# Performance work log

Hardware: AMD Instinct MI355X
Metric: run time of the kernel (lower is better)

## Reference

```python
import jax, jax.numpy as jnp
import numpy as np

MAX_DISP = 4  # matches init_kwargs


def setup_inputs() -> dict:
    key = jax.random.key(0)
    k1, k2 = jax.random.split(key)
    fmap1 = jax.random.normal(k1, (8, 256, 64, 128), dtype=jnp.float32)
    fmap2 = jax.random.normal(k2, (8, 256, 64, 128), dtype=jnp.float32)
    return {"fmap1": fmap1, "fmap2": fmap2}


def reference(fmap1, fmap2):
    # corr(x,y,dx,dy) = sum_c fmap1[c,y,x] * fmap2[c,y+dy,x+dx]
    pad = MAX_DISP
    B, C, H, W = fmap1.shape
    f2p = jnp.pad(fmap2, ((0, 0), (0, 0), (pad, pad), (pad, pad)))
    side = 2 * pad + 1  # 9 -> 81 displacements total
    # Loop over the small fixed set of 81 static displacements; each term is a
    # fused elementwise-multiply + channel reduction (einsum over c).
    corrs = [
        jnp.einsum('bchw,bchw->bhw', fmap1, f2p[:, :, y0:y0 + H, x0:x0 + W])
        for y0 in range(side)
        for x0 in range(side)
    ]
    return jnp.stack(corrs, axis=1)  # (B, 81, H, W)
```

## Files before the change

### kernel.cpp

```cpp
#include <hip/hip_runtime.h>


namespace {
constexpr int B_ = 8, C_ = 256, H_ = 64, W_ = 128;
constexpr int SIDE = 9, ND = 81, PAD = 4;
constexpr int HW = H_ * W_;
constexpr int CB = 32;
constexpr int HP = 72, WP = 144;
constexpr size_t BWS_U4 = (size_t)B_ * CB * HP * WP;
constexpr size_t BWS_BYTES = BWS_U4 * 16;
}

typedef __attribute__((ext_vector_type(8))) short short8;
typedef __attribute__((ext_vector_type(4))) float float4v;

__device__ __forceinline__ unsigned bf16rne(float f) {
  unsigned u = __float_as_uint(f);
  return (u + 0x7fffu + ((u >> 16) & 1u)) >> 16;
}
__device__ __forceinline__ unsigned packbf2(float lo, float hi) {
  return bf16rne(lo) | (bf16rne(hi) << 16);
}

__global__ __launch_bounds__(256)
void cvt_f2(const float* __restrict__ f2, uint4* __restrict__ bws) {
  const int tid = blockIdx.x * 256 + threadIdx.x;
  const int xq = tid % (WP / 4);
  int r = tid / (WP / 4);
  const int yp = r % HP;
  r /= HP;
  const int cb = r % CB;
  const int b = r / CB;

  uint4 o[4] = {};
  const int yg = yp - PAD;
  const int x = xq * 4 - PAD;
  if (yg >= 0 && yg < H_ && x >= 0 && x + 3 < W_) {
    const float* s = f2 + ((size_t)(b * C_ + cb * 8) * H_ + yg) * W_ + x;
    float vv[8][4];
#pragma unroll
    for (int e = 0; e < 8; ++e) {
      const float4 t = *(const float4*)(s + (size_t)e * HW);
      vv[e][0] = t.x; vv[e][1] = t.y; vv[e][2] = t.z; vv[e][3] = t.w;
    }
#pragma unroll
    for (int p = 0; p < 4; ++p) {
      o[p].x = packbf2(vv[0][p], vv[1][p]);
      o[p].y = packbf2(vv[2][p], vv[3][p]);
      o[p].z = packbf2(vv[4][p], vv[5][p]);
      o[p].w = packbf2(vv[6][p], vv[7][p]);
    }
  }
  uint4* d = bws + ((size_t)(b * CB + cb) * HP + yp) * WP + xq * 4;
#pragma unroll
  for (int p = 0; p < 4; ++p) d[p] = o[p];
}

__global__ __launch_bounds__(256, 4)
void corr_mfma(const float* __restrict__ f1, const uint4* __restrict__ bws,
               float* __restrict__ out) {
  const int t = threadIdx.x;
  const int lane = t & 63;
  const int wv = t >> 6;
  const int jm = blockIdx.x * 2 + (wv >> 1);
  const int half = wv & 1;
  const int y = blockIdx.y;
  const int b = blockIdx.z;
  const int v = lane & 15;
  const int q = lane >> 4;
  const int dyb = half * 5;
  const int ndy = 5 - half;

  float4v acc0[5], acc1[5];
#pragma unroll
  for (int i = 0; i < 5; ++i) {
    acc0[i] = (float4v){0.f, 0.f, 0.f, 0.f};
    acc1[i] = (float4v){0.f, 0.f, 0.f, 0.f};
  }

  const float* a_base = f1 + ((size_t)(b * C_ + q * 8) * H_ + y) * W_ + 16 * jm + v;
  const uint4* b_base = bws + ((size_t)(b * CB) + q) * (HP * WP) + 16 * jm + v;

  for (int ch = 0; ch < 8; ++ch) {
    float av[8];
#pragma unroll
    for (int j = 0; j < 8; ++j) av[j] = a_base[(size_t)(ch * 32 + j) * HW];
    uint4 afu;
    afu.x = packbf2(av[0], av[1]);
    afu.y = packbf2(av[2], av[3]);
    afu.z = packbf2(av[4], av[5]);
    afu.w = packbf2(av[6], av[7]);
    const short8 af = __builtin_bit_cast(short8, afu);

    const uint4* bc = b_base + (size_t)(ch * 4) * (HP * WP) + (size_t)(y + dyb) * WP;
#pragma unroll
    for (int i = 0; i < 5; ++i) {
      if (i < ndy) {
        const uint4* bp = bc + (size_t)i * WP;
        const short8 b0 = __builtin_bit_cast(short8, bp[0]);
        const short8 b1 = __builtin_bit_cast(short8, bp[16]);
        acc0[i] = __builtin_amdgcn_mfma_f32_16x16x32_bf16(af, b0, acc0[i], 0, 0, 0);
        acc1[i] = __builtin_amdgcn_mfma_f32_16x16x32_bf16(af, b1, acc1[i], 0, 0, 0);
      }
    }
  }

#pragma unroll
  for (int i = 0; i < 5; ++i) {
    if (i < ndy) {
      const int dy = dyb + i;
#pragma unroll
      for (int r = 0; r < 4; ++r) {
        const int m = q * 4 + r;
        const int x = 16 * jm + m;
        const int dx0 = v - m;
        if (dx0 >= 0 && dx0 <= 8)
          out[(((size_t)b * ND + dy * SIDE + dx0) * H_ + y) * W_ + x] = acc0[i][r];
        const int dx1 = v - m + 16;
        if (dx1 <= 8)
          out[(((size_t)b * ND + dy * SIDE + dx1) * H_ + y) * W_ + x] = acc1[i][r];
      }
    }
  }
}

namespace fb {
constexpr int PXS = 20, F2PX = 80, F1PX = 64, KC = 32, NCH = C_ / KC;
constexpr int F2U = SIDE * (F2PX / 4) * (KC / 2);
constexpr int F1U = (F1PX / 4) * (KC / 2);
constexpr int NU = F2U + F1U;
}

__global__ __launch_bounds__(512, 4)
void corr_fallback(const float* __restrict__ f1, const float* __restrict__ f2,
                   float* __restrict__ out) {
  using namespace fb;
  __shared__ __align__(16) unsigned f2s[SIDE * F2PX * PXS];
  __shared__ __align__(16) unsigned f1s[F1PX * PXS];

  const int t = threadIdx.x;
  const int bx = blockIdx.x, by = blockIdx.y, b = blockIdx.z;
  const int x0B = bx * 64;
  const int lane = t & 63, wv = t >> 6;
  const int wt = wv >> 1, half = wv & 1;
  const int dyb = half * 5, ndy = 5 - half;
  const int v = lane & 15, q = lane >> 4;

  float4v acc0[5], acc1[5];
#pragma unroll
  for (int i = 0; i < 5; ++i) {
    acc0[i] = (float4v){0.f, 0.f, 0.f, 0.f};
    acc1[i] = (float4v){0.f, 0.f, 0.f, 0.f};
  }
  const float* __restrict__ f1b = f1 + (size_t)b * C_ * HW;
  const float* __restrict__ f2b = f2 + (size_t)b * C_ * HW;

  for (int ch = 0; ch < NCH; ++ch) {
    const int c0 = ch * KC;
    if (ch) __syncthreads();
    for (int u = t; u < NU; u += 512) {
      if (u < F2U) {
        const int cp = u & 15;
        const int rp = u >> 4;
        const int pxq = rp % 20;
        const int r = rp / 20;
        const int yg = by + r - PAD;
        const int xb = x0B - PAD + pxq * 4;
        float4 va = make_float4(0.f, 0.f, 0.f, 0.f), vb = va;
        if (yg >= 0 && yg < H_ && xb >= 0 && xb <= W_ - 4) {
          const float* p = f2b + ((size_t)(c0 + 2 * cp) * H_ + yg) * W_ + xb;
          va = *(const float4*)p;
          vb = *(const float4*)(p + HW);
        }
        unsigned* d = &f2s[(r * F2PX + pxq * 4) * PXS + cp];
        d[0 * PXS] = packbf2(va.x, vb.x);
        d[1 * PXS] = packbf2(va.y, vb.y);
        d[2 * PXS] = packbf2(va.z, vb.z);
        d[3 * PXS] = packbf2(va.w, vb.w);
      } else {
        const int u2 = u - F2U;
        const int cp = u2 & 15;
        const int pxq = u2 >> 4;
        const float* p = f1b + ((size_t)(c0 + 2 * cp) * H_ + by) * W_ + x0B + pxq * 4;
        const float4 va = *(const float4*)p;
        const float4 vb = *(const float4*)(p + HW);
        unsigned* d = &f1s[(pxq * 4) * PXS + cp];
        d[0 * PXS] = packbf2(va.x, vb.x);
        d[1 * PXS] = packbf2(va.y, vb.y);
        d[2 * PXS] = packbf2(va.z, vb.z);
        d[3 * PXS] = packbf2(va.w, vb.w);
      }
    }
    __syncthreads();

    const short8 af =
        __builtin_bit_cast(short8, *(const uint4*)&f1s[(16 * wt + v) * PXS + 4 * q]);
#pragma unroll
    for (int i = 0; i < 5; ++i) {
      if (i < ndy) {
        const int dy = dyb + i;
        const unsigned* fbp = &f2s[(dy * F2PX + 16 * wt + v) * PXS + 4 * q];
        const short8 b0 = __builtin_bit_cast(short8, *(const uint4*)fbp);
        const short8 b1 = __builtin_bit_cast(short8, *(const uint4*)(fbp + 16 * PXS));
        acc0[i] = __builtin_amdgcn_mfma_f32_16x16x32_bf16(af, b0, acc0[i], 0, 0, 0);
        acc1[i] = __builtin_amdgcn_mfma_f32_16x16x32_bf16(af, b1, acc1[i], 0, 0, 0);
      }
    }
  }
#pragma unroll
  for (int i = 0; i < 5; ++i) {
    if (i < ndy) {
      const int dy = dyb + i;
#pragma unroll
      for (int r = 0; r < 4; ++r) {
        const int m = q * 4 + r;
        const int x = x0B + 16 * wt + m;
        const int dx0 = v - m;
        if (dx0 >= 0 && dx0 <= 8)
          out[(((size_t)b * ND + dy * SIDE + dx0) * H_ + by) * W_ + x] = acc0[i][r];
        const int dx1 = v - m + 16;
        if (dx1 <= 8)
          out[(((size_t)b * ND + dy * SIDE + dx1) * H_ + by) * W_ + x] = acc1[i][r];
      }
    }
  }
}

extern "C" void kernel_launch(void* const* d_in, const int* in_sizes, int n_in,
                              void* d_out, int out_size, void* d_ws, size_t ws_size,
                              hipStream_t stream) {
  const float* f1 = (const float*)d_in[0];
  const float* f2 = (const float*)d_in[1];
  float* out = (float*)d_out;

  if (ws_size >= BWS_BYTES) {
    uint4* bws = (uint4*)d_ws;
    const int n1 = (int)(BWS_U4 / 4);
    cvt_f2<<<dim3(n1 / 256), 256, 0, stream>>>(f2, bws);
    corr_mfma<<<dim3(4, H_, B_), 256, 0, stream>>>(f1, bws, out);
  } else {
    corr_fallback<<<dim3(2, H_, B_), 512, 0, stream>>>(f1, f2, out);
  }
}
```

Before: 216.5 us.

## Pre-convert both feature maps to bf16 and double-buffer MFMA operand loads

```diff
diff --git a/kernel.cpp b/kernel.cpp
--- a/kernel.cpp
+++ b/kernel.cpp
@@ -7,8 +7,9 @@
 constexpr int HW = H_ * W_;
 constexpr int CB = 32;
 constexpr int HP = 72, WP = 144;
-constexpr size_t BWS_U4 = (size_t)B_ * CB * HP * WP;
-constexpr size_t BWS_BYTES = BWS_U4 * 16;
+constexpr size_t NF2 = (size_t)B_ * CB * HP * WP;
+constexpr size_t NF1 = (size_t)B_ * CB * H_ * W_;
+constexpr size_t WS_BYTES = (NF2 + NF1) * 16;
 }
 
 typedef __attribute__((ext_vector_type(8))) short short8;
@@ -23,41 +24,46 @@
 }
 
 __global__ __launch_bounds__(256)
-void cvt_f2(const float* __restrict__ f2, uint4* __restrict__ bws) {
-  const int tid = blockIdx.x * 256 + threadIdx.x;
-  const int xq = tid % (WP / 4);
-  int r = tid / (WP / 4);
-  const int yp = r % HP;
-  r /= HP;
-  const int cb = r % CB;
-  const int b = r / CB;
-
-  uint4 o[4] = {};
-  const int yg = yp - PAD;
-  const int x = xq * 4 - PAD;
-  if (yg >= 0 && yg < H_ && x >= 0 && x + 3 < W_) {
-    const float* s = f2 + ((size_t)(b * C_ + cb * 8) * H_ + yg) * W_ + x;
-    float vv[8][4];
-#pragma unroll
-    for (int e = 0; e < 8; ++e) {
-      const float4 t = *(const float4*)(s + (size_t)e * HW);
-      vv[e][0] = t.x; vv[e][1] = t.y; vv[e][2] = t.z; vv[e][3] = t.w;
-    }
-#pragma unroll
-    for (int p = 0; p < 4; ++p) {
-      o[p].x = packbf2(vv[0][p], vv[1][p]);
-      o[p].y = packbf2(vv[2][p], vv[3][p]);
-      o[p].z = packbf2(vv[4][p], vv[5][p]);
-      o[p].w = packbf2(vv[6][p], vv[7][p]);
-    }
-  }
-  uint4* d = bws + ((size_t)(b * CB + cb) * HP + yp) * WP + xq * 4;
-#pragma unroll
-  for (int p = 0; p < 4; ++p) d[p] = o[p];
+void cvt_both(const float* __restrict__ f1, const float* __restrict__ f2,
+              uint4* __restrict__ w1, uint4* __restrict__ w2) {
+  const size_t tid = (size_t)blockIdx.x * 256 + threadIdx.x;
+  if (tid < NF2) {
+    const int xp = (int)(tid % WP);
+    size_t r = tid / WP;
+    const int yp = (int)(r % HP);
+    r /= HP;
+    const int cb = (int)(r % CB);
+    const int b = (int)(r / CB);
+    const int yg = yp - PAD, xg = xp - PAD;
+    uint4 o = {0u, 0u, 0u, 0u};
+    if (yg >= 0 && yg < H_ && xg >= 0 && xg < W_) {
+      const float* s = f2 + ((size_t)(b * C_ + cb * 8) * H_ + yg) * W_ + xg;
+      o.x = packbf2(s[0 * HW], s[1 * HW]);
+      o.y = packbf2(s[2 * HW], s[3 * HW]);
+      o.z = packbf2(s[4 * HW], s[5 * HW]);
+      o.w = packbf2(s[6 * HW], s[7 * HW]);
+    }
+    w2[tid] = o;
+  } else {
+    const size_t t2 = tid - NF2;
+    const int x = (int)(t2 % W_);
+    size_t r = t2 / W_;
+    const int y = (int)(r % H_);
+    r /= H_;
+    const int cb = (int)(r % CB);
+    const int b = (int)(r / CB);
+    const float* s = f1 + ((size_t)(b * C_ + cb * 8) * H_ + y) * W_ + x;
+    uint4 o;
+    o.x = packbf2(s[0 * HW], s[1 * HW]);
+    o.y = packbf2(s[2 * HW], s[3 * HW]);
+    o.z = packbf2(s[4 * HW], s[5 * HW]);
+    o.w = packbf2(s[6 * HW], s[7 * HW]);
+    w1[t2] = o;
+  }
 }
 
 __global__ __launch_bounds__(256, 4)
-void corr_mfma(const float* __restrict__ f1, const uint4* __restrict__ bws,
+void corr_mfma(const uint4* __restrict__ w1, const uint4* __restrict__ w2,
                float* __restrict__ out) {
   const int t = threadIdx.x;
   const int lane = t & 63;
@@ -78,29 +84,39 @@
     acc1[i] = (float4v){0.f, 0.f, 0.f, 0.f};
   }
 
-  const float* a_base = f1 + ((size_t)(b * C_ + q * 8) * H_ + y) * W_ + 16 * jm + v;
-  const uint4* b_base = bws + ((size_t)(b * CB) + q) * (HP * WP) + 16 * jm + v;
-
-  for (int ch = 0; ch < 8; ++ch) {
-    float av[8];
-#pragma unroll
-    for (int j = 0; j < 8; ++j) av[j] = a_base[(size_t)(ch * 32 + j) * HW];
-    uint4 afu;
-    afu.x = packbf2(av[0], av[1]);
-    afu.y = packbf2(av[2], av[3]);
-    afu.z = packbf2(av[4], av[5]);
-    afu.w = packbf2(av[6], av[7]);
-    const short8 af = __builtin_bit_cast(short8, afu);
-
-    const uint4* bc = b_base + (size_t)(ch * 4) * (HP * WP) + (size_t)(y + dyb) * WP;
+  const uint4* a_base =
+      w1 + ((size_t)(b * CB + q) * H_ + y) * W_ + 16 * jm + v;
+  const uint4* b_base =
+      w2 + ((size_t)(b * CB + q) * HP + (y + dyb)) * WP + 16 * jm + v;
+
+  uint4 A[2];
+  uint4 Bv[2][10];
+
+  auto load_chunk = [&](int ch, int s) {
+    A[s] = a_base[(size_t)ch * 4 * (H_ * W_)];
+    const uint4* bc = b_base + (size_t)ch * 4 * (HP * WP);
 #pragma unroll
     for (int i = 0; i < 5; ++i) {
       if (i < ndy) {
-        const uint4* bp = bc + (size_t)i * WP;
-        const short8 b0 = __builtin_bit_cast(short8, bp[0]);
-        const short8 b1 = __builtin_bit_cast(short8, bp[16]);
-        acc0[i] = __builtin_amdgcn_mfma_f32_16x16x32_bf16(af, b0, acc0[i], 0, 0, 0);
-        acc1[i] = __builtin_amdgcn_mfma_f32_16x16x32_bf16(af, b1, acc1[i], 0, 0, 0);
+        Bv[s][2 * i] = bc[(size_t)i * WP];
+        Bv[s][2 * i + 1] = bc[(size_t)i * WP + 16];
+      }
+    }
+  };
+
+  load_chunk(0, 0);
+#pragma unroll
+  for (int ch = 0; ch < 8; ++ch) {
+    const int s = ch & 1;
+    if (ch < 7) load_chunk(ch + 1, s ^ 1);
+    const short8 af = __builtin_bit_cast(short8, A[s]);
+#pragma unroll
+    for (int i = 0; i < 5; ++i) {
+      if (i < ndy) {
+        acc0[i] = __builtin_amdgcn_mfma_f32_16x16x32_bf16(
+            af, __builtin_bit_cast(short8, Bv[s][2 * i]), acc0[i], 0, 0, 0);
+        acc1[i] = __builtin_amdgcn_mfma_f32_16x16x32_bf16(
+            af, __builtin_bit_cast(short8, Bv[s][2 * i + 1]), acc1[i], 0, 0, 0);
       }
     }
   }
@@ -233,11 +249,12 @@
   const float* f2 = (const float*)d_in[1];
   float* out = (float*)d_out;
 
-  if (ws_size >= BWS_BYTES) {
-    uint4* bws = (uint4*)d_ws;
-    const int n1 = (int)(BWS_U4 / 4);
-    cvt_f2<<<dim3(n1 / 256), 256, 0, stream>>>(f2, bws);
-    corr_mfma<<<dim3(4, H_, B_), 256, 0, stream>>>(f1, bws, out);
+  if (ws_size >= WS_BYTES) {
+    uint4* w2 = (uint4*)d_ws;
+    uint4* w1 = w2 + NF2;
+    const int nthreads = (int)(NF2 + NF1);
+    cvt_both<<<dim3(nthreads / 256), 256, 0, stream>>>(f1, f2, w1, w2);
+    corr_mfma<<<dim3(4, H_, B_), 256, 0, stream>>>(w1, w2, out);
   } else {
     corr_fallback<<<dim3(2, H_, B_), 512, 0, stream>>>(f1, f2, out);
   }
```

After: 228.9 us. 5.8% more time.

## Tile correlation as 4x4 spatial patches with split-K across two waves

Applied to the files above, without the earlier changes.

```diff
diff --git a/kernel.cpp b/kernel.cpp
--- a/kernel.cpp
+++ b/kernel.cpp
@@ -7,8 +7,8 @@
 constexpr int HW = H_ * W_;
 constexpr int CB = 32;
 constexpr int HP = 72, WP = 144;
-constexpr size_t BWS_U4 = (size_t)B_ * CB * HP * WP;
-constexpr size_t BWS_BYTES = BWS_U4 * 16;
+constexpr size_t NW2 = (size_t)B_ * CB * HP * WP;
+constexpr size_t WS_BYTES = NW2 * 16;
 }
 
 typedef __attribute__((ext_vector_type(8))) short short8;
@@ -56,35 +56,44 @@
   for (int p = 0; p < 4; ++p) d[p] = o[p];
 }
 
-__global__ __launch_bounds__(256, 4)
-void corr_mfma(const float* __restrict__ f1, const uint4* __restrict__ bws,
+__global__ __launch_bounds__(128, 4)
+void corr_mfma(const float* __restrict__ f1, const uint4* __restrict__ w2,
                float* __restrict__ out) {
+  __shared__ float red[36 * 64];
+
   const int t = threadIdx.x;
   const int lane = t & 63;
-  const int wv = t >> 6;
-  const int jm = blockIdx.x * 2 + (wv >> 1);
-  const int half = wv & 1;
-  const int y = blockIdx.y;
-  const int b = blockIdx.z;
+  const int cs = t >> 6;
   const int v = lane & 15;
   const int q = lane >> 4;
-  const int dyb = half * 5;
-  const int ndy = 5 - half;
-
-  float4v acc0[5], acc1[5];
-#pragma unroll
-  for (int i = 0; i < 5; ++i) {
-    acc0[i] = (float4v){0.f, 0.f, 0.f, 0.f};
-    acc1[i] = (float4v){0.f, 0.f, 0.f, 0.f};
-  }
-
-  const float* a_base = f1 + ((size_t)(b * C_ + q * 8) * H_ + y) * W_ + 16 * jm + v;
-  const uint4* b_base = bws + ((size_t)(b * CB) + q) * (HP * WP) + 16 * jm + v;
-
-  for (int ch = 0; ch < 8; ++ch) {
+  const int Ax = blockIdx.x * 4;
+  const int Ay = blockIdx.y * 4;
+  const int b = blockIdx.z;
+
+  const int ya = Ay + (v >> 2);
+  const int xa = Ax + (v & 3);
+
+  float4v acc[9];
+#pragma unroll
+  for (int k = 0; k < 9; ++k) acc[k] = (float4v){0.f, 0.f, 0.f, 0.f};
+
+  const float* a0 =
+      f1 + ((size_t)(b * C_ + cs * 128 + q * 8) * H_ + ya) * W_ + xa;
+  const uint4* b0 =
+      w2 + ((size_t)(b * CB + cs * 16 + q) * HP + Ay + (v >> 2)) * WP + Ax + (v & 3);
+
+  for (int ch = 0; ch < 4; ++ch) {
+    uint4 Bv[9];
+    const uint4* bp = b0 + (size_t)(ch * 4) * (HP * WP);
+#pragma unroll
+    for (int i = 0; i < 3; ++i)
+#pragma unroll
+      for (int j = 0; j < 3; ++j)
+        Bv[3 * i + j] = bp[(size_t)(4 * i) * WP + 4 * j];
+
     float av[8];
 #pragma unroll
-    for (int j = 0; j < 8; ++j) av[j] = a_base[(size_t)(ch * 32 + j) * HW];
+    for (int j = 0; j < 8; ++j) av[j] = a0[(size_t)(ch * 32 + j) * HW];
     uint4 afu;
     afu.x = packbf2(av[0], av[1]);
     afu.y = packbf2(av[2], av[3]);
@@ -92,35 +101,39 @@
     afu.w = packbf2(av[6], av[7]);
     const short8 af = __builtin_bit_cast(short8, afu);
 
-    const uint4* bc = b_base + (size_t)(ch * 4) * (HP * WP) + (size_t)(y + dyb) * WP;
-#pragma unroll
-    for (int i = 0; i < 5; ++i) {
-      if (i < ndy) {
-        const uint4* bp = bc + (size_t)i * WP;
-        const short8 b0 = __builtin_bit_cast(short8, bp[0]);
-        const short8 b1 = __builtin_bit_cast(short8, bp[16]);
-        acc0[i] = __builtin_amdgcn_mfma_f32_16x16x32_bf16(af, b0, acc0[i], 0, 0, 0);
-        acc1[i] = __builtin_amdgcn_mfma_f32_16x16x32_bf16(af, b1, acc1[i], 0, 0, 0);
-      }
-    }
-  }
-
-#pragma unroll
-  for (int i = 0; i < 5; ++i) {
-    if (i < ndy) {
-      const int dy = dyb + i;
-#pragma unroll
-      for (int r = 0; r < 4; ++r) {
-        const int m = q * 4 + r;
-        const int x = 16 * jm + m;
-        const int dx0 = v - m;
-        if (dx0 >= 0 && dx0 <= 8)
-          out[(((size_t)b * ND + dy * SIDE + dx0) * H_ + y) * W_ + x] = acc0[i][r];
-        const int dx1 = v - m + 16;
-        if (dx1 <= 8)
-          out[(((size_t)b * ND + dy * SIDE + dx1) * H_ + y) * W_ + x] = acc1[i][r];
-      }
-    }
+#pragma unroll
+    for (int k = 0; k < 9; ++k)
+      acc[k] = __builtin_amdgcn_mfma_f32_16x16x32_bf16(
+          af, __builtin_bit_cast(short8, Bv[k]), acc[k], 0, 0, 0);
+  }
+
+  if (cs == 1) {
+#pragma unroll
+    for (int k = 0; k < 9; ++k)
+#pragma unroll
+      for (int r = 0; r < 4; ++r) red[(k * 4 + r) * 64 + lane] = acc[k][r];
+  }
+  __syncthreads();
+  if (cs == 0) {
+#pragma unroll
+    for (int k = 0; k < 9; ++k)
+#pragma unroll
+      for (int r = 0; r < 4; ++r) acc[k][r] += red[(k * 4 + r) * 64 + lane];
+
+#pragma unroll
+    for (int i = 0; i < 3; ++i)
+#pragma unroll
+      for (int j = 0; j < 3; ++j)
+#pragma unroll
+        for (int r = 0; r < 4; ++r) {
+          const int m = q * 4 + r;
+          const int dy = 4 * i + (v >> 2) - (m >> 2);
+          const int dx = 4 * j + (v & 3) - (m & 3);
+          if (dy >= 0 && dy <= 8 && dx >= 0 && dx <= 8) {
+            out[((size_t)(b * ND + dy * SIDE + dx) * H_ + Ay + (m >> 2)) * W_ +
+                Ax + (m & 3)] = acc[3 * i + j][r];
+          }
+        }
   }
 }
 
@@ -233,11 +246,11 @@
   const float* f2 = (const float*)d_in[1];
   float* out = (float*)d_out;
 
-  if (ws_size >= BWS_BYTES) {
-    uint4* bws = (uint4*)d_ws;
-    const int n1 = (int)(BWS_U4 / 4);
-    cvt_f2<<<dim3(n1 / 256), 256, 0, stream>>>(f2, bws);
-    corr_mfma<<<dim3(4, H_, B_), 256, 0, stream>>>(f1, bws, out);
+  if (ws_size >= WS_BYTES) {
+    uint4* w2 = (uint4*)d_ws;
+    const int n1 = (int)(NW2 / 4);
+    cvt_f2<<<dim3(n1 / 256), 256, 0, stream>>>(f2, w2);
+    corr_mfma<<<dim3(W_ / 4, H_ / 4, B_), 128, 0, stream>>>(f1, w2, out);
   } else {
     corr_fallback<<<dim3(2, H_, B_), 512, 0, stream>>>(f1, f2, out);
   }
```

Measured after the change: 269.1 us. 24.3% more time.

## Interleave batches across blocks, one-pixel cvt threads, and prefetch B operands

Applied to the files above, without the earlier changes.

```diff
diff --git a/kernel.cpp b/kernel.cpp
--- a/kernel.cpp
+++ b/kernel.cpp
@@ -7,8 +7,9 @@
 constexpr int HW = H_ * W_;
 constexpr int CB = 32;
 constexpr int HP = 72, WP = 144;
-constexpr size_t BWS_U4 = (size_t)B_ * CB * HP * WP;
-constexpr size_t BWS_BYTES = BWS_U4 * 16;
+constexpr size_t NW2 = (size_t)B_ * CB * HP * WP;
+constexpr size_t WS_BYTES = NW2 * 16;
+constexpr int PERB = (int)(NW2 / B_);
 }
 
 typedef __attribute__((ext_vector_type(8))) short short8;
@@ -23,49 +24,41 @@
 }
 
 __global__ __launch_bounds__(256)
-void cvt_f2(const float* __restrict__ f2, uint4* __restrict__ bws) {
-  const int tid = blockIdx.x * 256 + threadIdx.x;
-  const int xq = tid % (WP / 4);
-  int r = tid / (WP / 4);
+void cvt_f2(const float* __restrict__ f2, uint4* __restrict__ w2) {
+  const int id = blockIdx.x;
+  const int b = id & 7;
+  const int e = (id >> 3) * 256 + threadIdx.x;
+  const int xp = e % WP;
+  const int r = e / WP;
   const int yp = r % HP;
-  r /= HP;
-  const int cb = r % CB;
-  const int b = r / CB;
-
-  uint4 o[4] = {};
-  const int yg = yp - PAD;
-  const int x = xq * 4 - PAD;
-  if (yg >= 0 && yg < H_ && x >= 0 && x + 3 < W_) {
-    const float* s = f2 + ((size_t)(b * C_ + cb * 8) * H_ + yg) * W_ + x;
-    float vv[8][4];
-#pragma unroll
-    for (int e = 0; e < 8; ++e) {
-      const float4 t = *(const float4*)(s + (size_t)e * HW);
-      vv[e][0] = t.x; vv[e][1] = t.y; vv[e][2] = t.z; vv[e][3] = t.w;
-    }
-#pragma unroll
-    for (int p = 0; p < 4; ++p) {
-      o[p].x = packbf2(vv[0][p], vv[1][p]);
-      o[p].y = packbf2(vv[2][p], vv[3][p]);
-      o[p].z = packbf2(vv[4][p], vv[5][p]);
-      o[p].w = packbf2(vv[6][p], vv[7][p]);
-    }
-  }
-  uint4* d = bws + ((size_t)(b * CB + cb) * HP + yp) * WP + xq * 4;
-#pragma unroll
-  for (int p = 0; p < 4; ++p) d[p] = o[p];
+  const int cb = r / HP;
+
+  const int yg = yp - PAD, xg = xp - PAD;
+  uint4 o = {0u, 0u, 0u, 0u};
+  if (yg >= 0 && yg < H_ && xg >= 0 && xg < W_) {
+    const float* s = f2 + ((size_t)(b * C_ + cb * 8) * H_ + yg) * W_ + xg;
+    o.x = packbf2(s[0 * HW], s[1 * HW]);
+    o.y = packbf2(s[2 * HW], s[3 * HW]);
+    o.z = packbf2(s[4 * HW], s[5 * HW]);
+    o.w = packbf2(s[6 * HW], s[7 * HW]);
+  }
+  w2[(size_t)b * PERB + e] = o;
 }
 
 __global__ __launch_bounds__(256, 4)
-void corr_mfma(const float* __restrict__ f1, const uint4* __restrict__ bws,
+void corr_mfma(const float* __restrict__ f1, const uint4* __restrict__ w2,
                float* __restrict__ out) {
+  const int id = blockIdx.x;
+  const int b = id & 7;
+  const int k = id >> 3;
+  const int bx = k & 3;
+  const int y = k >> 2;
+
   const int t = threadIdx.x;
   const int lane = t & 63;
   const int wv = t >> 6;
-  const int jm = blockIdx.x * 2 + (wv >> 1);
+  const int jm = bx * 2 + (wv >> 1);
   const int half = wv & 1;
-  const int y = blockIdx.y;
-  const int b = blockIdx.z;
   const int v = lane & 15;
   const int q = lane >> 4;
   const int dyb = half * 5;
@@ -78,10 +71,22 @@
     acc1[i] = (float4v){0.f, 0.f, 0.f, 0.f};
   }
 
-  const float* a_base = f1 + ((size_t)(b * C_ + q * 8) * H_ + y) * W_ + 16 * jm + v;
-  const uint4* b_base = bws + ((size_t)(b * CB) + q) * (HP * WP) + 16 * jm + v;
-
+  const float* a_base =
+      f1 + ((size_t)(b * C_ + q * 8) * H_ + y) * W_ + 16 * jm + v;
+  const uint4* b_base =
+      w2 + ((size_t)(b * CB + q) * HP + (y + dyb)) * WP + 16 * jm + v;
+
+#pragma unroll
   for (int ch = 0; ch < 8; ++ch) {
+    uint4 Bv[10];
+    const uint4* bc = b_base + (size_t)(ch * 4) * (HP * WP);
+#pragma unroll
+    for (int i = 0; i < 5; ++i) {
+      if (i < ndy) {
+        Bv[2 * i] = bc[(size_t)i * WP];
+        Bv[2 * i + 1] = bc[(size_t)i * WP + 16];
+      }
+    }
     float av[8];
 #pragma unroll
     for (int j = 0; j < 8; ++j) av[j] = a_base[(size_t)(ch * 32 + j) * HW];
@@ -92,15 +97,13 @@
     afu.w = packbf2(av[6], av[7]);
     const short8 af = __builtin_bit_cast(short8, afu);
 
-    const uint4* bc = b_base + (size_t)(ch * 4) * (HP * WP) + (size_t)(y + dyb) * WP;
 #pragma unroll
     for (int i = 0; i < 5; ++i) {
       if (i < ndy) {
-        const uint4* bp = bc + (size_t)i * WP;
-        const short8 b0 = __builtin_bit_cast(short8, bp[0]);
-        const short8 b1 = __builtin_bit_cast(short8, bp[16]);
-        acc0[i] = __builtin_amdgcn_mfma_f32_16x16x32_bf16(af, b0, acc0[i], 0, 0, 0);
-        acc1[i] = __builtin_amdgcn_mfma_f32_16x16x32_bf16(af, b1, acc1[i], 0, 0, 0);
+        acc0[i] = __builtin_amdgcn_mfma_f32_16x16x32_bf16(
+            af, __builtin_bit_cast(short8, Bv[2 * i]), acc0[i], 0, 0, 0);
+        acc1[i] = __builtin_amdgcn_mfma_f32_16x16x32_bf16(
+            af, __builtin_bit_cast(short8, Bv[2 * i + 1]), acc1[i], 0, 0, 0);
       }
     }
   }
@@ -233,11 +236,10 @@
   const float* f2 = (const float*)d_in[1];
   float* out = (float*)d_out;
 
-  if (ws_size >= BWS_BYTES) {
-    uint4* bws = (uint4*)d_ws;
-    const int n1 = (int)(BWS_U4 / 4);
-    cvt_f2<<<dim3(n1 / 256), 256, 0, stream>>>(f2, bws);
-    corr_mfma<<<dim3(4, H_, B_), 256, 0, stream>>>(f1, bws, out);
+  if (ws_size >= WS_BYTES) {
+    uint4* w2 = (uint4*)d_ws;
+    cvt_f2<<<dim3((int)(NW2 / 256)), 256, 0, stream>>>(f2, w2);
+    corr_mfma<<<dim3(2048), 256, 0, stream>>>(f1, w2, out);
   } else {
     corr_fallback<<<dim3(2, H_, B_), 512, 0, stream>>>(f1, f2, out);
   }
```

Measured after the change: 214.0 us. Within noise of the previous version (-1.1%).
